# Kernel optimization log

Hardware: AMD Instinct MI355X
Metric: run time of the kernel (lower is better)

The kernel has to match this reference:

```python
import jax, jax.numpy as jnp
import numpy as np

H = 2048      # hidden_size
DM = 4096     # intermediate_size
N = 16        # ssm state size
K = 4         # conv kernel
R = 128       # time_step_rank
B_SZ = 1
L = 1024


def setup_inputs() -> dict:
    key = jax.random.key(0)
    ks = jax.random.split(key, 10)
    s = 0.02
    hidden_states = jax.random.normal(ks[0], (B_SZ, L, H), dtype=jnp.float32)
    W_in = jax.random.normal(ks[1], (2 * DM, H), dtype=jnp.float32) * s
    conv_w = jax.random.normal(ks[2], (DM, 1, K), dtype=jnp.float32) * 0.3
    conv_b = jax.random.normal(ks[3], (DM,), dtype=jnp.float32) * 0.1
    W_x = jax.random.normal(ks[4], (R + 2 * N, DM), dtype=jnp.float32) * s
    W_dt = jax.random.normal(ks[5], (DM, R), dtype=jnp.float32) * s
    b_dt = jax.random.normal(ks[6], (DM,), dtype=jnp.float32) * 0.1
    # A_log init: log(arange(1..N)) broadcast over channels (per __init__)
    A_log = jnp.broadcast_to(jnp.log(jnp.arange(1, N + 1, dtype=jnp.float32))[None, :], (DM, N)).copy()
    D_param = jnp.ones((DM,), dtype=jnp.float32)
    W_out = jax.random.normal(ks[7], (H, DM), dtype=jnp.float32) * s
    return {"hidden_states": hidden_states, "W_in": W_in, "conv_w": conv_w,
            "conv_b": conv_b, "W_x": W_x, "W_dt": W_dt, "b_dt": b_dt,
            "A_log": A_log, "D_param": D_param, "W_out": W_out}


def reference(hidden_states, W_in, conv_w, conv_b, W_x, W_dt, b_dt, A_log, D_param, W_out):
    # in_proj then chunk into hidden / gate (torch chunks dim=1 after transpose)
    proj = hidden_states @ W_in.T                     # [B, L, 2D]
    h, gate = proj[..., :DM], proj[..., DM:]          # each [B, L, D]
    # depthwise causal conv1d, padding K-1 then truncate to L (left-pad == same)
    h_cl = jnp.transpose(h, (0, 2, 1))                # [B, D, L]
    hc = jax.lax.conv_general_dilated(
        h_cl, conv_w, window_strides=(1,), padding=[(K - 1, 0)],
        dimension_numbers=("NCH", "OIH", "NCH"), feature_group_count=DM)
    hc = jax.nn.silu(hc + conv_b[None, :, None])      # [B, D, L]
    hc_ld = jnp.transpose(hc, (0, 2, 1))              # [B, L, D]
    # x_proj -> dt, B, C
    ssm_p = hc_ld @ W_x.T                             # [B, L, R+2N]
    ts, Bm, Cm = ssm_p[..., :R], ssm_p[..., R:R + N], ssm_p[..., R + N:]
    dt = jax.nn.softplus(ts @ W_dt.T + b_dt)          # [B, L, D]
    A = -jnp.exp(A_log)                               # [D, N]
    dA = jnp.exp(dt[:, :, :, None] * A[None, None, :, :])            # [B, L, D, N]
    dBu = dt[:, :, :, None] * Bm[:, :, None, :] * hc_ld[:, :, :, None]  # [B, L, D, N]
    # selective scan over time: state = dA*state + dBu; y = <state, C>
    def step(state, inp):
        dA_t, dBu_t, C_t = inp                        # [B,D,N],[B,D,N],[B,N]
        state = dA_t * state + dBu_t
        y = jnp.einsum("bdn,bn->bd", state, C_t)
        return state, y
    init = jnp.zeros((hidden_states.shape[0], DM, N), dtype=hidden_states.dtype)
    _, ys = jax.lax.scan(step, init,
                         (jnp.swapaxes(dA, 0, 1), jnp.swapaxes(dBu, 0, 1), jnp.swapaxes(Cm, 0, 1)))
    y = jnp.transpose(ys, (1, 0, 2))                  # [B, L, D]
    y = y + hc_ld * D_param[None, None, :]            # skip via D
    y = y * jax.nn.silu(gate)                         # gating
    return y @ W_out.T                                # [B, L, H]
```

## Files before the change

### kernel.cpp

```cpp
#include <hip/hip_runtime.h>
#include <math.h>

#define AS1 __attribute__((address_space(1)))
#define AS3 __attribute__((address_space(3)))

typedef __attribute__((ext_vector_type(8))) short short8;
typedef __attribute__((ext_vector_type(8))) unsigned short ushort8_t;
typedef __attribute__((ext_vector_type(4))) float f32x4;

#define WAITV(n) asm volatile("s_waitcnt vmcnt(" #n ")" ::: "memory")
#define BARRIER() asm volatile("s_barrier" ::: "memory")

static __device__ __forceinline__ unsigned short f2bf(float f) {
    unsigned u = __float_as_uint(f);
    unsigned r = (u + 0x7fffu + ((u >> 16) & 1u)) >> 16;
    return (unsigned short)r;
}
static __device__ __forceinline__ float bf2f(unsigned short u) {
    return __uint_as_float(((unsigned)u) << 16);
}

__global__ __launch_bounds__(256) void cvt_f32_bf16(const float* __restrict__ src,
                                                    unsigned short* __restrict__ dst,
                                                    int n4) {
    int i = blockIdx.x * 256 + threadIdx.x;
    int stride = gridDim.x * 256;
    for (; i < n4; i += stride) {
        float4 v = ((const float4*)src)[i];
        ushort4 o;
        o.x = f2bf(v.x); o.y = f2bf(v.y); o.z = f2bf(v.z); o.w = f2bf(v.w);
        ((ushort4*)dst)[i] = o;
    }
}

__global__ __launch_bounds__(256) void cvt_ts(const float* __restrict__ ssmp,
                                              unsigned short* __restrict__ ts) {
    int i = blockIdx.x * 256 + threadIdx.x;
    int t = i >> 5, c4 = (i & 31) * 4;
    float4 v = *(const float4*)&ssmp[t * 160 + c4];
    ushort4 o;
    o.x = f2bf(v.x); o.y = f2bf(v.y); o.z = f2bf(v.z); o.w = f2bf(v.w);
    *(ushort4*)&ts[t * 128 + c4] = o;
}

__global__ __launch_bounds__(256) void conv_silu(const unsigned short* __restrict__ h,
                                                 const float* __restrict__ cw,
                                                 const float* __restrict__ cb,
                                                 unsigned short* __restrict__ hc_bf) {
    int idx = blockIdx.x * 256 + threadIdx.x;
    int d = idx & 4095, t = idx >> 12;
    float acc = cb[d];
    float4 w = *(const float4*)&cw[d * 4];
    const float* wp = (const float*)&w;
#pragma unroll
    for (int k = 0; k < 4; ++k) {
        int tt = t + k - 3;
        if (tt >= 0) acc += bf2f(h[tt * 4096 + d]) * wp[k];
    }
    float s = acc / (1.f + __expf(-acc));
    hc_bf[idx] = f2bf(s);
}

__global__ __launch_bounds__(256) void reduce2(const unsigned short* __restrict__ P,
                                               unsigned short* __restrict__ h_bf,
                                               unsigned short* __restrict__ gate_bf) {
    const int NCHK = 1024 * 8192 / 8;
    int i = blockIdx.x * 256 + threadIdx.x;
    int stride = gridDim.x * 256;
    for (; i < NCHK; i += stride) {
        ushort8_t a = ((const ushort8_t*)P)[i];
        ushort8_t b = ((const ushort8_t*)P)[i + NCHK];
        int e0 = i * 8;
        int row = e0 >> 13, col = e0 & 8191;
        ushort8_t o;
        if (col < 4096) {
#pragma unroll
            for (int j = 0; j < 8; ++j) o[j] = f2bf(bf2f(a[j]) + bf2f(b[j]));
            ((ushort8_t*)h_bf)[(row * 4096 + col) >> 3] = o;
        } else {
#pragma unroll
            for (int j = 0; j < 8; ++j) {
                float v = bf2f(a[j]) + bf2f(b[j]);
                o[j] = f2bf(v / (1.f + __expf(-v)));
            }
            ((ushort8_t*)gate_bf)[(row * 4096 + (col - 4096)) >> 3] = o;
        }
    }
}

__global__ __launch_bounds__(256) void reduce8(const unsigned short* __restrict__ P,
                                               float* __restrict__ out) {
    const int NCHK = 1024 * 2048 / 4;
    int i = blockIdx.x * 256 + threadIdx.x;
    int stride = gridDim.x * 256;
    for (; i < NCHK; i += stride) {
        float4 s = make_float4(0.f, 0.f, 0.f, 0.f);
#pragma unroll
        for (int z = 0; z < 8; ++z) {
            ushort4 v = ((const ushort4*)(P + (size_t)z * 1024 * 2048))[i];
            s.x += bf2f(v.x); s.y += bf2f(v.y); s.z += bf2f(v.z); s.w += bf2f(v.w);
        }
        ((float4*)out)[i] = s;
    }
}

__global__ __launch_bounds__(512, 2)
void gemm256p(const short* __restrict__ A, const short* __restrict__ B,
              unsigned short* __restrict__ Pbase,
              int N, int K, int kchunk) {
    __shared__ short lds[3 * 16384];

    const int tid = threadIdx.x;
    const int wv = tid >> 6, ln = tid & 63;
    const int lr = ln & 15, kg = ln >> 4;
    const int wm = wv >> 2, wn = wv & 3;

    const int nwg = gridDim.x;
    const int bid = blockIdx.x;
    const int swz = (bid & 7) * (nwg >> 3) + (bid >> 3);
    const int by = swz & 3, bx = swz >> 2;
    const int m0 = by * 256, n0 = bx * 256;
    const int kbeg = blockIdx.z * kchunk;
    const int NT = kchunk >> 5;

    f32x4 acc[8][4];
#pragma unroll
    for (int mi = 0; mi < 8; ++mi)
#pragma unroll
        for (int ni = 0; ni < 4; ++ni) acc[mi][ni] = (f32x4){0.f, 0.f, 0.f, 0.f};

    const short* Abase = A + (size_t)m0 * K + kbeg;
    const short* Bbase = B + (size_t)n0 * K + kbeg;

#define STG(gbase, ldsoff, kt, b, pass)                                       \
    {                                                                         \
        int c = (pass) * 512 + tid;                                           \
        int row = c >> 2, ch = (c & 3) * 8;                                   \
        const short* src = (gbase) + (size_t)row * K + (kt) * 32 + ch;        \
        short* dst = &lds[(b) * 16384 + (ldsoff) + ((pass) * 512 + wv * 64) * 8]; \
        __builtin_amdgcn_global_load_lds((const AS1 void*)src,                \
                                         (AS3 void*)dst, 16, 0, 0);           \
    }
#define STAGE_A(kt, b) { STG(Abase, 0, kt, b, 0); STG(Abase, 0, kt, b, 1); }
#define STAGE_B(kt, b) { STG(Bbase, 8192, kt, b, 0); STG(Bbase, 8192, kt, b, 1); }
#define RD_A(dst, mi)                                                         \
    { int row = wm * 128 + (mi) * 16 + lr;                                    \
      dst = *(const short8*)&la[row * 32 + kg * 8]; }
#define RD_B(dst, ni)                                                         \
    { int row = wn * 64 + (ni) * 16 + lr;                                     \
      dst = *(const short8*)&lb[row * 32 + kg * 8]; }
#define MFMA4(mi, a)                                                          \
    acc[mi][0] = __builtin_amdgcn_mfma_f32_16x16x32_bf16(a, vb0, acc[mi][0], 0, 0, 0); \
    acc[mi][1] = __builtin_amdgcn_mfma_f32_16x16x32_bf16(a, vb1, acc[mi][1], 0, 0, 0); \
    acc[mi][2] = __builtin_amdgcn_mfma_f32_16x16x32_bf16(a, vb2, acc[mi][2], 0, 0, 0); \
    acc[mi][3] = __builtin_amdgcn_mfma_f32_16x16x32_bf16(a, vb3, acc[mi][3], 0, 0, 0);

    STAGE_A(0, 0); STAGE_B(0, 0);
    STAGE_A(1, 1); STAGE_B(1, 1);

    int b = 0;
    for (int kt = 0; kt < NT; ++kt) {
        if (kt + 1 < NT) { WAITV(4); } else { WAITV(0); }
        BARRIER();
        int bn = b + 2; if (bn >= 3) bn -= 3;
        if (kt + 2 < NT) STAGE_A(kt + 2, bn);

        const short* la = &lds[b * 16384];
        const short* lb = la + 8192;
        short8 va0, va1, va2, va3, vb0, vb1, vb2, vb3;
        RD_B(vb0, 0); RD_B(vb1, 1); RD_B(vb2, 2); RD_B(vb3, 3);
        RD_A(va0, 0); RD_A(va1, 1); RD_A(va2, 2); RD_A(va3, 3);
        __builtin_amdgcn_s_setprio(1);
        MFMA4(0, va0); MFMA4(1, va1); MFMA4(2, va2); MFMA4(3, va3);
        __builtin_amdgcn_s_setprio(0);
        BARRIER();
        if (kt + 2 < NT) STAGE_B(kt + 2, bn);
        RD_A(va0, 4); RD_A(va1, 5); RD_A(va2, 6); RD_A(va3, 7);
        __builtin_amdgcn_s_setprio(1);
        MFMA4(4, va0); MFMA4(5, va1); MFMA4(6, va2); MFMA4(7, va3);
        __builtin_amdgcn_s_setprio(0);
        b = (b + 1 == 3) ? 0 : b + 1;
    }
#undef STG
#undef STAGE_A
#undef STAGE_B
#undef RD_A
#undef RD_B
#undef MFMA4

    unsigned short* P = Pbase + (size_t)blockIdx.z * 1024 * N;
#pragma unroll
    for (int mi = 0; mi < 8; ++mi) {
        int crow0 = m0 + wm * 128 + mi * 16 + kg * 4;
#pragma unroll
        for (int ni = 0; ni < 4; ++ni) {
            int ccol = n0 + wn * 64 + ni * 16 + lr;
#pragma unroll
            for (int i = 0; i < 4; ++i)
                P[(size_t)(crow0 + i) * N + ccol] = f2bf(acc[mi][ni][i]);
        }
    }
}

enum { EPI_PLAIN = 0, EPI_SPLIT = 1, EPI_ATOMIC = 2, EPI_SOFTPLUS = 3 };

template <int BM, int EPI>
__global__ __launch_bounds__(256)
void gemm_bt(const short* __restrict__ A, const short* __restrict__ B,
             float* __restrict__ C, float* __restrict__ C2,
             const float* __restrict__ bias,
             int M, int N, int K, int ldc, int kcLen) {
    __shared__ short A_lds[BM * 32];
    __shared__ short B_lds[128 * 32];
    const int tid = threadIdx.x;
    const int wv = tid >> 6, ln = tid & 63;
    const int lr = ln & 15, kg = ln >> 4;
    const int m0 = blockIdx.y * BM;
    const int n0 = blockIdx.x * 128;
    const int kbeg = blockIdx.z * kcLen;
    const int kend = kbeg + kcLen;
    const int wm = wv >> 1, wn = wv & 1;
    constexpr int MR = BM / 32;

    f32x4 acc[MR][4];
#pragma unroll
    for (int mi = 0; mi < MR; ++mi)
#pragma unroll
        for (int ni = 0; ni < 4; ++ni) acc[mi][ni] = (f32x4){0.f, 0.f, 0.f, 0.f};

    const int arow = tid >> 2;
    const int kq8 = (tid & 3) * 8;

    for (int k0 = kbeg; k0 < kend; k0 += 32) {
#pragma unroll
        for (int r = 0; r < BM / 64; ++r) {
            const short* srcA = A + (size_t)(m0 + r * 64 + arow) * K + (k0 + kq8);
            short* dstA = &A_lds[(r * 64 + wv * 16) * 32];
            __builtin_amdgcn_global_load_lds((const AS1 void*)srcA, (AS3 void*)dstA, 16, 0, 0);
        }
#pragma unroll
        for (int r = 0; r < 2; ++r) {
            int brow = n0 + r * 64 + arow;
            if (brow > N - 1) brow = N - 1;
            const short* srcB = B + (size_t)brow * K + (k0 + kq8);
            short* dstB = &B_lds[(r * 64 + wv * 16) * 32];
            __builtin_amdgcn_global_load_lds((const AS1 void*)srcB, (AS3 void*)dstB, 16, 0, 0);
        }
        __syncthreads();

        short8 av[MR], bv[4];
#pragma unroll
        for (int mi = 0; mi < MR; ++mi)
            av[mi] = *(const short8*)&A_lds[(wm * (BM / 2) + mi * 16 + lr) * 32 + kg * 8];
#pragma unroll
        for (int ni = 0; ni < 4; ++ni)
            bv[ni] = *(const short8*)&B_lds[(wn * 64 + ni * 16 + lr) * 32 + kg * 8];
#pragma unroll
        for (int mi = 0; mi < MR; ++mi)
#pragma unroll
            for (int ni = 0; ni < 4; ++ni)
                acc[mi][ni] = __builtin_amdgcn_mfma_f32_16x16x32_bf16(av[mi], bv[ni], acc[mi][ni], 0, 0, 0);
        __syncthreads();
    }

#pragma unroll
    for (int mi = 0; mi < MR; ++mi) {
        int crow0 = m0 + wm * (BM / 2) + mi * 16 + kg * 4;
#pragma unroll
        for (int ni = 0; ni < 4; ++ni) {
            int ccol = n0 + wn * 64 + ni * 16 + lr;
#pragma unroll
            for (int i = 0; i < 4; ++i) {
                float v = acc[mi][ni][i];
                size_t crow = (size_t)(crow0 + i);
                if constexpr (EPI == EPI_PLAIN) {
                    C[crow * ldc + ccol] = v;
                } else if constexpr (EPI == EPI_SPLIT) {
                    if (ccol < 4096) C[crow * 4096 + ccol] = v;
                    else C2[crow * 4096 + (ccol - 4096)] = v;
                } else if constexpr (EPI == EPI_ATOMIC) {
                    if (ccol < N) atomicAdd(&C[crow * ldc + ccol], v);
                } else {
                    float x = v + bias[ccol];
                    float sp = fmaxf(x, 0.f) + log1pf(__expf(-fabsf(x)));
                    ((unsigned short*)C)[crow * ldc + ccol] = f2bf(sp);
                }
            }
        }
    }
}

#define CLEN 16
#define NCH 64

__global__ __launch_bounds__(256)
void scan_p1(const unsigned short* __restrict__ dt, const unsigned short* __restrict__ hc,
             const float* __restrict__ ssmp, const float* __restrict__ A_log,
             float* __restrict__ Sbuf, float* __restrict__ dtsum) {
    const int tid = threadIdx.x;
    const int c = blockIdx.x & (NCH - 1);
    const int db = blockIdx.x >> 6;
    const int d = db * 256 + tid;
    const int t0 = c * CLEN;

    float Ac[16];
#pragma unroll
    for (int i = 0; i < 4; ++i) {
        float4 v = *(const float4*)&A_log[d * 16 + i * 4];
        Ac[i*4+0] = -__expf(v.x); Ac[i*4+1] = -__expf(v.y);
        Ac[i*4+2] = -__expf(v.z); Ac[i*4+3] = -__expf(v.w);
    }

    __shared__ float sB[CLEN][16];
    sB[tid >> 4][tid & 15] = ssmp[(t0 + (tid >> 4)) * 160 + 128 + (tid & 15)];
    __syncthreads();

    float st[16];
#pragma unroll
    for (int n = 0; n < 16; ++n) st[n] = 0.f;
    float ds = 0.f;

    for (int tt = 0; tt < CLEN; ++tt) {
        size_t g = (size_t)(t0 + tt) * 4096 + d;
        float dtv = bf2f(dt[g]);
        float hcv = bf2f(hc[g]);
        float du = dtv * hcv;
        ds += dtv;
#pragma unroll
        for (int n = 0; n < 16; ++n) {
            float dA = __expf(dtv * Ac[n]);
            st[n] = fmaf(dA, st[n], du * sB[tt][n]);
        }
    }

    float* o = Sbuf + ((size_t)c * 4096 + d) * 16;
#pragma unroll
    for (int i = 0; i < 4; ++i)
        *(float4*)&o[i * 4] = make_float4(st[i*4], st[i*4+1], st[i*4+2], st[i*4+3]);
    dtsum[c * 4096 + d] = ds;
}

__global__ __launch_bounds__(256)
void scan_p2(const float* __restrict__ A_log, const float* __restrict__ dtsum,
             float* __restrict__ S) {
    const int idx = blockIdx.x * 256 + threadIdx.x;
    const int d = idx >> 4;
    const float Ac = -__expf(A_log[idx]);

    float sl[NCH], Pv[NCH];
#pragma unroll
    for (int c = 0; c < NCH; ++c) sl[c] = S[(size_t)c * 65536 + idx];
#pragma unroll
    for (int c = 0; c < NCH; ++c) Pv[c] = __expf(Ac * dtsum[c * 4096 + d]);

    float s = 0.f;
#pragma unroll
    for (int c = 0; c < NCH; ++c) {
        S[(size_t)c * 65536 + idx] = s;
        s = fmaf(Pv[c], s, sl[c]);
    }
}

__global__ __launch_bounds__(256)
void scan_p3(const unsigned short* __restrict__ dt, const unsigned short* __restrict__ hc,
             const float* __restrict__ ssmp, const float* __restrict__ A_log,
             const float* __restrict__ Dp, const unsigned short* __restrict__ gate,
             const float* __restrict__ Sinit, unsigned short* __restrict__ y_bf) {
    const int tid = threadIdx.x;
    const int c = blockIdx.x & (NCH - 1);
    const int db = blockIdx.x >> 6;
    const int d = db * 256 + tid;
    const int t0 = c * CLEN;

    float Ac[16];
#pragma unroll
    for (int i = 0; i < 4; ++i) {
        float4 v = *(const float4*)&A_log[d * 16 + i * 4];
        Ac[i*4+0] = -__expf(v.x); Ac[i*4+1] = -__expf(v.y);
        Ac[i*4+2] = -__expf(v.z); Ac[i*4+3] = -__expf(v.w);
    }
    const float Dcoef = Dp[d];

    __shared__ float sB[CLEN][16], sC[CLEN][16];
    {
        int tt = tid >> 4, nn = tid & 15;
        sB[tt][nn] = ssmp[(t0 + tt) * 160 + 128 + nn];
        sC[tt][nn] = ssmp[(t0 + tt) * 160 + 144 + nn];
    }
    __syncthreads();

    float st[16];
    {
        const float* si = Sinit + ((size_t)c * 4096 + d) * 16;
#pragma unroll
        for (int i = 0; i < 4; ++i) {
            float4 v = *(const float4*)&si[i * 4];
            st[i*4] = v.x; st[i*4+1] = v.y; st[i*4+2] = v.z; st[i*4+3] = v.w;
        }
    }

    for (int tt = 0; tt < CLEN; ++tt) {
        size_t g = (size_t)(t0 + tt) * 4096 + d;
        float dtv = bf2f(dt[g]);
        float hcv = bf2f(hc[g]);
        float du = dtv * hcv;
        float p[16];
#pragma unroll
        for (int n = 0; n < 16; ++n) {
            float dA = __expf(dtv * Ac[n]);
            st[n] = fmaf(dA, st[n], du * sB[tt][n]);
            p[n] = st[n] * sC[tt][n];
        }
#pragma unroll
        for (int n = 0; n < 8; ++n) p[n] += p[n + 8];
#pragma unroll
        for (int n = 0; n < 4; ++n) p[n] += p[n + 4];
        p[0] += p[2]; p[1] += p[3];
        float csum = p[0] + p[1];
        float gv = bf2f(gate[g]);
        float yv = (csum + hcv * Dcoef) * gv;
        y_bf[g] = f2bf(yv);
    }
}

extern "C" void kernel_launch(void* const* d_in, const int* in_sizes, int n_in,
                              void* d_out, int out_size, void* d_ws, size_t ws_size,
                              hipStream_t stream) {
    (void)in_sizes; (void)n_in; (void)out_size; (void)ws_size;
    const float* hidden = (const float*)d_in[0];
    const float* W_in   = (const float*)d_in[1];
    const float* conv_w = (const float*)d_in[2];
    const float* conv_b = (const float*)d_in[3];
    const float* W_x    = (const float*)d_in[4];
    const float* W_dt   = (const float*)d_in[5];
    const float* b_dt   = (const float*)d_in[6];
    const float* A_log  = (const float*)d_in[7];
    const float* D_p    = (const float*)d_in[8];
    const float* W_out  = (const float*)d_in[9];
    float* out = (float*)d_out;

    char* w = (char*)d_ws;
    unsigned short* hid_bf = (unsigned short*)w;  w += (size_t)1024 * 2048 * 2;
    unsigned short* Wbig   = (unsigned short*)w;  w += (size_t)8192 * 2048 * 2;
    unsigned short* h_bf   = (unsigned short*)w;  w += (size_t)1024 * 4096 * 2;
    unsigned short* gate_bf= (unsigned short*)w;  w += (size_t)1024 * 4096 * 2;
    unsigned short* pscr   = (unsigned short*)w;  w += (size_t)16 * 1024 * 1024 * 2;
    unsigned short* hc_bf  = pscr;
    unsigned short* dt_bf  = pscr + (size_t)1024 * 4096;
    float* Sbuf            = (float*)(pscr + (size_t)2 * 1024 * 4096);
    float* ssmp            = (float*)w;           w += (size_t)1024 * 160 * 4;
    unsigned short* ts_bf  = (unsigned short*)w;  w += (size_t)1024 * 128 * 2;
    unsigned short* Wx_bf  = (unsigned short*)w;  w += (size_t)160 * 4096 * 2;
    unsigned short* Wdt_bf = (unsigned short*)w;  w += (size_t)4096 * 128 * 2;
    unsigned short* y_bf   = (unsigned short*)w;  w += (size_t)1024 * 4096 * 2;
    float* dtsum           = (float*)w;           w += (size_t)NCH * 4096 * 4;

    hipMemsetAsync(ssmp, 0, (size_t)1024 * 160 * 4, stream);

    cvt_f32_bf16<<<2048, 256, 0, stream>>>(hidden, hid_bf, 1024 * 2048 / 4);
    cvt_f32_bf16<<<4096, 256, 0, stream>>>(W_in, Wbig, 8192 * 2048 / 4);
    cvt_f32_bf16<<<640, 256, 0, stream>>>(W_x, Wx_bf, 160 * 4096 / 4);
    cvt_f32_bf16<<<512, 256, 0, stream>>>(W_dt, Wdt_bf, 4096 * 128 / 4);

    gemm256p<<<dim3(128, 1, 2), 512, 0, stream>>>(
        (const short*)hid_bf, (const short*)Wbig, pscr, 8192, 2048, 1024);
    reduce2<<<2048, 256, 0, stream>>>(pscr, h_bf, gate_bf);

    conv_silu<<<16384, 256, 0, stream>>>(h_bf, conv_w, conv_b, hc_bf);

    cvt_f32_bf16<<<2048, 256, 0, stream>>>(W_out, Wbig, 2048 * 4096 / 4);

    gemm_bt<128, EPI_ATOMIC><<<dim3(2, 8, 16), 256, 0, stream>>>(
        (const short*)hc_bf, (const short*)Wx_bf, ssmp, nullptr, nullptr,
        1024, 160, 4096, 160, 256);

    cvt_ts<<<128, 256, 0, stream>>>(ssmp, ts_bf);

    gemm_bt<128, EPI_SOFTPLUS><<<dim3(32, 8, 1), 256, 0, stream>>>(
        (const short*)ts_bf, (const short*)Wdt_bf, (float*)dt_bf, nullptr, b_dt,
        1024, 4096, 128, 4096, 128);

    scan_p1<<<NCH * 16, 256, 0, stream>>>(dt_bf, hc_bf, ssmp, A_log, Sbuf, dtsum);
    scan_p2<<<256, 256, 0, stream>>>(A_log, dtsum, Sbuf);
    scan_p3<<<NCH * 16, 256, 0, stream>>>(dt_bf, hc_bf, ssmp, A_log, D_p, gate_bf, Sbuf, y_bf);

    gemm256p<<<dim3(32, 1, 8), 512, 0, stream>>>(
        (const short*)y_bf, (const short*)Wbig, pscr, 2048, 4096, 512);
    reduce8<<<2048, 256, 0, stream>>>(pscr, out);
}
```

Measured before the change: 227.8 us.

## Swizzle GEMM LDS layout, unroll triple-buffer loop, fuse weight conversions into one launch

The gemm256p kernel now XOR-swizzles the 16-byte chunk index by row when staging into LDS and when reading fragments. This is meant to cut LDS bank conflicts on the short8 reads. The main loop is unrolled by three so buffer indices are compile-time constants, and the global source pointers and LDS read offsets are precomputed and incremented instead of recomputed each step. Separately, the five fp32-to-bf16 conversions are merged into a single launch with a separate W_out buffer. This removes several kernel launches at the cost of extra workspace and a branchy index mapping.

```diff
diff --git a/kernel.cpp b/kernel.cpp
--- a/kernel.cpp
+++ b/kernel.cpp
@@ -20,16 +20,26 @@
     return __uint_as_float(((unsigned)u) << 16);
 }
 
-__global__ __launch_bounds__(256) void cvt_f32_bf16(const float* __restrict__ src,
-                                                    unsigned short* __restrict__ dst,
-                                                    int n4) {
+__global__ __launch_bounds__(256)
+void cvt_all(const float* __restrict__ s0, unsigned short* __restrict__ d0, int n0,
+             const float* __restrict__ s1, unsigned short* __restrict__ d1, int n1,
+             const float* __restrict__ s2, unsigned short* __restrict__ d2, int n2,
+             const float* __restrict__ s3, unsigned short* __restrict__ d3, int n3,
+             const float* __restrict__ s4, unsigned short* __restrict__ d4, int n4c) {
     int i = blockIdx.x * 256 + threadIdx.x;
     int stride = gridDim.x * 256;
-    for (; i < n4; i += stride) {
-        float4 v = ((const float4*)src)[i];
+    int t01 = n0 + n1, t02 = t01 + n2, t03 = t02 + n3, tot = t03 + n4c;
+    for (; i < tot; i += stride) {
+        const float* s; unsigned short* d; int j;
+        if (i < n0)      { s = s0; d = d0; j = i; }
+        else if (i < t01){ s = s1; d = d1; j = i - n0; }
+        else if (i < t02){ s = s2; d = d2; j = i - t01; }
+        else if (i < t03){ s = s3; d = d3; j = i - t02; }
+        else             { s = s4; d = d4; j = i - t03; }
+        float4 v = ((const float4*)s)[j];
         ushort4 o;
         o.x = f2bf(v.x); o.y = f2bf(v.y); o.z = f2bf(v.z); o.w = f2bf(v.w);
-        ((ushort4*)dst)[i] = o;
+        ((ushort4*)d)[j] = o;
     }
 }
 
@@ -129,64 +139,98 @@
 #pragma unroll
         for (int ni = 0; ni < 4; ++ni) acc[mi][ni] = (f32x4){0.f, 0.f, 0.f, 0.f};
 
-    const short* Abase = A + (size_t)m0 * K + kbeg;
-    const short* Bbase = B + (size_t)n0 * K + kbeg;
-
-#define STG(gbase, ldsoff, kt, b, pass)                                       \
-    {                                                                         \
-        int c = (pass) * 512 + tid;                                           \
-        int row = c >> 2, ch = (c & 3) * 8;                                   \
-        const short* src = (gbase) + (size_t)row * K + (kt) * 32 + ch;        \
-        short* dst = &lds[(b) * 16384 + (ldsoff) + ((pass) * 512 + wv * 64) * 8]; \
-        __builtin_amdgcn_global_load_lds((const AS1 void*)src,                \
-                                         (AS3 void*)dst, 16, 0, 0);           \
-    }
-#define STAGE_A(kt, b) { STG(Abase, 0, kt, b, 0); STG(Abase, 0, kt, b, 1); }
-#define STAGE_B(kt, b) { STG(Bbase, 8192, kt, b, 0); STG(Bbase, 8192, kt, b, 1); }
-#define RD_A(dst, mi)                                                         \
-    { int row = wm * 128 + (mi) * 16 + lr;                                    \
-      dst = *(const short8*)&la[row * 32 + kg * 8]; }
-#define RD_B(dst, ni)                                                         \
-    { int row = wn * 64 + (ni) * 16 + lr;                                     \
-      dst = *(const short8*)&lb[row * 32 + kg * 8]; }
+    const short *sA0, *sA1, *sB0, *sB1;
+    {
+        int c0 = tid,        r0 = c0 >> 2, ss0 = (c0 & 3) ^ ((r0 >> 1) & 3);
+        int c1 = 512 + tid,  r1 = c1 >> 2, ss1 = (c1 & 3) ^ ((r1 >> 1) & 3);
+        sA0 = A + (size_t)(m0 + r0) * K + kbeg + ss0 * 8;
+        sA1 = A + (size_t)(m0 + r1) * K + kbeg + ss1 * 8;
+        sB0 = B + (size_t)(n0 + r0) * K + kbeg + ss0 * 8;
+        sB1 = B + (size_t)(n0 + r1) * K + kbeg + ss1 * 8;
+    }
+    const int dA0 = wv * 512;
+    const int dA1 = 4096 + wv * 512;
+    const int dB0 = 8192 + wv * 512;
+    const int dB1 = 12288 + wv * 512;
+    int roA[8], roB[4];
+#pragma unroll
+    for (int mi = 0; mi < 8; ++mi) {
+        int row = wm * 128 + mi * 16 + lr;
+        roA[mi] = row * 32 + (kg ^ ((row >> 1) & 3)) * 8;
+    }
+#pragma unroll
+    for (int ni = 0; ni < 4; ++ni) {
+        int row = wn * 64 + ni * 16 + lr;
+        roB[ni] = 8192 + row * 32 + (kg ^ ((row >> 1) & 3)) * 8;
+    }
+
+#define STAGE_A(BB)                                                           \
+    { __builtin_amdgcn_global_load_lds((const AS1 void*)sA0,                  \
+          (AS3 void*)(lds + (BB) * 16384 + dA0), 16, 0, 0);                   \
+      __builtin_amdgcn_global_load_lds((const AS1 void*)sA1,                  \
+          (AS3 void*)(lds + (BB) * 16384 + dA1), 16, 0, 0);                   \
+      sA0 += 32; sA1 += 32; }
+#define STAGE_B(BB)                                                           \
+    { __builtin_amdgcn_global_load_lds((const AS1 void*)sB0,                  \
+          (AS3 void*)(lds + (BB) * 16384 + dB0), 16, 0, 0);                   \
+      __builtin_amdgcn_global_load_lds((const AS1 void*)sB1,                  \
+          (AS3 void*)(lds + (BB) * 16384 + dB1), 16, 0, 0);                   \
+      sB0 += 32; sB1 += 32; }
 #define MFMA4(mi, a)                                                          \
     acc[mi][0] = __builtin_amdgcn_mfma_f32_16x16x32_bf16(a, vb0, acc[mi][0], 0, 0, 0); \
     acc[mi][1] = __builtin_amdgcn_mfma_f32_16x16x32_bf16(a, vb1, acc[mi][1], 0, 0, 0); \
     acc[mi][2] = __builtin_amdgcn_mfma_f32_16x16x32_bf16(a, vb2, acc[mi][2], 0, 0, 0); \
     acc[mi][3] = __builtin_amdgcn_mfma_f32_16x16x32_bf16(a, vb3, acc[mi][3], 0, 0, 0);
 
-    STAGE_A(0, 0); STAGE_B(0, 0);
-    STAGE_A(1, 1); STAGE_B(1, 1);
-
-    int b = 0;
-    for (int kt = 0; kt < NT; ++kt) {
-        if (kt + 1 < NT) { WAITV(4); } else { WAITV(0); }
-        BARRIER();
-        int bn = b + 2; if (bn >= 3) bn -= 3;
-        if (kt + 2 < NT) STAGE_A(kt + 2, bn);
-
-        const short* la = &lds[b * 16384];
-        const short* lb = la + 8192;
-        short8 va0, va1, va2, va3, vb0, vb1, vb2, vb3;
-        RD_B(vb0, 0); RD_B(vb1, 1); RD_B(vb2, 2); RD_B(vb3, 3);
-        RD_A(va0, 0); RD_A(va1, 1); RD_A(va2, 2); RD_A(va3, 3);
-        __builtin_amdgcn_s_setprio(1);
-        MFMA4(0, va0); MFMA4(1, va1); MFMA4(2, va2); MFMA4(3, va3);
-        __builtin_amdgcn_s_setprio(0);
-        BARRIER();
-        if (kt + 2 < NT) STAGE_B(kt + 2, bn);
-        RD_A(va0, 4); RD_A(va1, 5); RD_A(va2, 6); RD_A(va3, 7);
-        __builtin_amdgcn_s_setprio(1);
-        MFMA4(4, va0); MFMA4(5, va1); MFMA4(6, va2); MFMA4(7, va3);
-        __builtin_amdgcn_s_setprio(0);
-        b = (b + 1 == 3) ? 0 : b + 1;
-    }
-#undef STG
+#define BODY(BB, BN2, ktv)                                                    \
+    {                                                                         \
+        if ((ktv) + 1 < NT) { WAITV(4); } else { WAITV(0); }                  \
+        BARRIER();                                                            \
+        const bool pf_ = (ktv) + 2 < NT;                                      \
+        if (pf_) STAGE_A(BN2);                                                \
+        const short* la = lds + (BB) * 16384;                                 \
+        short8 va0, va1, va2, va3, vb0, vb1, vb2, vb3;                        \
+        vb0 = *(const short8*)(la + roB[0]);                                  \
+        vb1 = *(const short8*)(la + roB[1]);                                  \
+        vb2 = *(const short8*)(la + roB[2]);                                  \
+        vb3 = *(const short8*)(la + roB[3]);                                  \
+        va0 = *(const short8*)(la + roA[0]);                                  \
+        va1 = *(const short8*)(la + roA[1]);                                  \
+        va2 = *(const short8*)(la + roA[2]);                                  \
+        va3 = *(const short8*)(la + roA[3]);                                  \
+        __builtin_amdgcn_s_setprio(1);                                        \
+        MFMA4(0, va0); MFMA4(1, va1); MFMA4(2, va2); MFMA4(3, va3);           \
+        __builtin_amdgcn_s_setprio(0);                                        \
+        BARRIER();                                                            \
+        if (pf_) STAGE_B(BN2);                                                \
+        va0 = *(const short8*)(la + roA[4]);                                  \
+        va1 = *(const short8*)(la + roA[5]);                                  \
+        va2 = *(const short8*)(la + roA[6]);                                  \
+        va3 = *(const short8*)(la + roA[7]);                                  \
+        __builtin_amdgcn_s_setprio(1);                                        \
+        MFMA4(4, va0); MFMA4(5, va1); MFMA4(6, va2); MFMA4(7, va3);           \
+        __builtin_amdgcn_s_setprio(0);                                        \
+    }
+
+    STAGE_A(0); STAGE_B(0);
+    STAGE_A(1); STAGE_B(1);
+
+    int kt = 0;
+    for (; kt + 3 <= NT; kt += 3) {
+        BODY(0, 2, kt);
+        BODY(1, 0, kt + 1);
+        BODY(2, 1, kt + 2);
+    }
+    for (; kt < NT; ++kt) {
+        int bb = kt % 3;
+        if (bb == 0)      BODY(0, 2, kt)
+        else if (bb == 1) BODY(1, 0, kt)
+        else              BODY(2, 1, kt)
+    }
 #undef STAGE_A
 #undef STAGE_B
-#undef RD_A
-#undef RD_B
 #undef MFMA4
+#undef BODY
 
     unsigned short* P = Pbase + (size_t)blockIdx.z * 1024 * N;
 #pragma unroll
@@ -442,6 +486,7 @@
     char* w = (char*)d_ws;
     unsigned short* hid_bf = (unsigned short*)w;  w += (size_t)1024 * 2048 * 2;
     unsigned short* Wbig   = (unsigned short*)w;  w += (size_t)8192 * 2048 * 2;
+    unsigned short* Wout_bf= (unsigned short*)w;  w += (size_t)2048 * 4096 * 2;
     unsigned short* h_bf   = (unsigned short*)w;  w += (size_t)1024 * 4096 * 2;
     unsigned short* gate_bf= (unsigned short*)w;  w += (size_t)1024 * 4096 * 2;
     unsigned short* pscr   = (unsigned short*)w;  w += (size_t)16 * 1024 * 1024 * 2;
@@ -457,10 +502,12 @@
 
     hipMemsetAsync(ssmp, 0, (size_t)1024 * 160 * 4, stream);
 
-    cvt_f32_bf16<<<2048, 256, 0, stream>>>(hidden, hid_bf, 1024 * 2048 / 4);
-    cvt_f32_bf16<<<4096, 256, 0, stream>>>(W_in, Wbig, 8192 * 2048 / 4);
-    cvt_f32_bf16<<<640, 256, 0, stream>>>(W_x, Wx_bf, 160 * 4096 / 4);
-    cvt_f32_bf16<<<512, 256, 0, stream>>>(W_dt, Wdt_bf, 4096 * 128 / 4);
+    cvt_all<<<4096, 256, 0, stream>>>(
+        hidden, hid_bf, 1024 * 2048 / 4,
+        W_in, Wbig, 8192 * 2048 / 4,
+        W_x, Wx_bf, 160 * 4096 / 4,
+        W_dt, Wdt_bf, 4096 * 128 / 4,
+        W_out, Wout_bf, 2048 * 4096 / 4);
 
     gemm256p<<<dim3(128, 1, 2), 512, 0, stream>>>(
         (const short*)hid_bf, (const short*)Wbig, pscr, 8192, 2048, 1024);
@@ -468,8 +515,6 @@
 
     conv_silu<<<16384, 256, 0, stream>>>(h_bf, conv_w, conv_b, hc_bf);
 
-    cvt_f32_bf16<<<2048, 256, 0, stream>>>(W_out, Wbig, 2048 * 4096 / 4);
-
     gemm_bt<128, EPI_ATOMIC><<<dim3(2, 8, 16), 256, 0, stream>>>(
         (const short*)hc_bf, (const short*)Wx_bf, ssmp, nullptr, nullptr,
         1024, 160, 4096, 160, 256);
@@ -485,6 +530,6 @@
     scan_p3<<<NCH * 16, 256, 0, stream>>>(dt_bf, hc_bf, ssmp, A_log, D_p, gate_bf, Sbuf, y_bf);
 
     gemm256p<<<dim3(32, 1, 8), 512, 0, stream>>>(
-        (const short*)y_bf, (const short*)Wbig, pscr, 2048, 4096, 512);
+        (const short*)y_bf, (const short*)Wout_bf, pscr, 2048, 4096, 512);
     reduce8<<<2048, 256, 0, stream>>>(pscr, out);
 }
```

New measurement: 248.9 us. 9.3% more time.
